# Performance work log

Hardware: AMD Instinct MI355X
Metric: run time of the kernel (lower is better)

Reference implementation:

```python
import jax, jax.numpy as jnp
import numpy as np

EMB = 1024
HEADS = 16
HEAD_DIM = EMB // HEADS
EPS = 1e-5


def setup_inputs() -> dict:
    key = jax.random.key(0)
    ks = jax.random.split(key, 10)
    B, T, D = 2, 2048, EMB
    s = 1.0 / np.sqrt(D)
    inp = {
        "x": jax.random.normal(ks[0], (B, T, D), dtype=jnp.float32),
        "wq": jax.random.normal(ks[1], (D, D), dtype=jnp.float32) * s,
        "bq": jnp.zeros((D,), jnp.float32),
        "wk": jax.random.normal(ks[2], (D, D), dtype=jnp.float32) * s,
        "bk": jnp.zeros((D,), jnp.float32),
        "wv": jax.random.normal(ks[3], (D, D), dtype=jnp.float32) * s,
        "bv": jnp.zeros((D,), jnp.float32),
        "wo": jax.random.normal(ks[4], (D, D), dtype=jnp.float32) * s,
        "bo": jnp.zeros((D,), jnp.float32),
        "gamma": jnp.ones((D,), jnp.float32),
        "beta": jnp.zeros((D,), jnp.float32),
    }
    return inp


def _attention(x, wq, bq, wk, bk, wv, bv, wo, bo, gamma, beta):
    B, T, D = x.shape
    H, Hd = HEADS, HEAD_DIM
    q = (x @ wq + bq).reshape(B, T, H, Hd)
    k = (x @ wk + bk).reshape(B, T, H, Hd)
    v = (x @ wv + bv).reshape(B, T, H, Hd)
    # scores: [B, H, T, T]
    scores = jnp.einsum("bthd,bshd->bhts", q, k) / np.sqrt(Hd)
    attn = jax.nn.softmax(scores, axis=-1)  # dropout is identity in eval
    ctx = jnp.einsum("bhts,bshd->bthd", attn, v).reshape(B, T, D)
    out = ctx @ wo + bo
    y = x + out  # residual (dropout identity)
    mu = jnp.mean(y, axis=-1, keepdims=True)
    var = jnp.var(y, axis=-1, keepdims=True)
    return (y - mu) * jax.lax.rsqrt(var + EPS) * gamma + beta


def reference(x, wq, bq, wk, bk, wv, bv, wo, bo, gamma, beta):
    return _attention(x, wq, bq, wk, bk, wv, bv, wo, bo, gamma, beta)
```

## Files before the change

kernel.cpp:

```cpp
#include <hip/hip_runtime.h>

#define BSZ   2
#define TSEQ  2048
#define DMOD  1024
#define NHEAD 16
#define HDIM  64
#define MROW  (BSZ*TSEQ)
#define LNEPS 1e-5f
#define QSCALE 0.18033688011f

typedef __bf16 bf16x8 __attribute__((ext_vector_type(8)));
typedef float  f32x4  __attribute__((ext_vector_type(4)));
typedef unsigned short us8 __attribute__((ext_vector_type(8)));
typedef unsigned short us4 __attribute__((ext_vector_type(4)));

__device__ __forceinline__ unsigned short f2bf(float f) {
    unsigned u = __float_as_uint(f);
    u += 0x7FFF + ((u >> 16) & 1);
    return (unsigned short)(u >> 16);
}
__device__ __forceinline__ float bf2f(unsigned short u) {
    return __uint_as_float((unsigned)u << 16);
}

__device__ __forceinline__ float fexp2(float x) {
#if __has_builtin(__builtin_amdgcn_exp2f)
    return __builtin_amdgcn_exp2f(x);
#else
    return __expf(x * 0.6931471805599453f);
#endif
}

__device__ __forceinline__ void gld_lds16(const void* g, void* l) {
    __builtin_amdgcn_global_load_lds(
        (const __attribute__((address_space(1))) unsigned int*)g,
        (__attribute__((address_space(3))) unsigned int*)l, 16, 0, 0);
}

__global__ __launch_bounds__(256) void prep_k(
    const float* __restrict__ x,
    const float* __restrict__ wq, const float* __restrict__ wk,
    const float* __restrict__ wv, const float* __restrict__ wo,
    unsigned short* __restrict__ Xb,
    unsigned short* __restrict__ WqkvT, unsigned short* __restrict__ WoT)
{
    const int tid = threadIdx.x;
    if (blockIdx.x < 2048) {
        const size_t i = ((size_t)blockIdx.x * 256 + tid) * 8;
        float4 a = *(const float4*)&x[i];
        float4 b = *(const float4*)&x[i + 4];
        union { unsigned short u[8]; uint4 v; } o;
        o.u[0]=f2bf(a.x); o.u[1]=f2bf(a.y); o.u[2]=f2bf(a.z); o.u[3]=f2bf(a.w);
        o.u[4]=f2bf(b.x); o.u[5]=f2bf(b.y); o.u[6]=f2bf(b.z); o.u[7]=f2bf(b.w);
        *(uint4*)&Xb[i] = o.v;
        return;
    }
    __shared__ float T[64][68];
    const int id = blockIdx.x - 2048;
    const int z  = id >> 8;
    const int bx = id & 15;
    const int by = (id >> 4) & 15;
    const float* W = (z == 0) ? wq : (z == 1) ? wk : (z == 2) ? wv : wo;
    unsigned short* Wt = (z < 3) ? (WqkvT + (size_t)z*1024*1024) : WoT;
    const int lr = tid >> 4, lc = (tid & 15) * 4;
    #pragma unroll
    for (int p = 0; p < 4; ++p) {
        const int kk = p*16 + lr;
        float4 v = *(const float4*)&W[(size_t)(by*64 + kk)*1024 + bx*64 + lc];
        T[lc+0][kk] = v.x; T[lc+1][kk] = v.y; T[lc+2][kk] = v.z; T[lc+3][kk] = v.w;
    }
    __syncthreads();
    #pragma unroll
    for (int p = 0; p < 2; ++p) {
        const int nl = p*32 + (tid >> 3);
        const int kb = (tid & 7) * 8;
        float4 a = *(const float4*)&T[nl][kb];
        float4 b = *(const float4*)&T[nl][kb+4];
        union { unsigned short u[8]; uint4 v; } o;
        o.u[0]=f2bf(a.x); o.u[1]=f2bf(a.y); o.u[2]=f2bf(a.z); o.u[3]=f2bf(a.w);
        o.u[4]=f2bf(b.x); o.u[5]=f2bf(b.y); o.u[6]=f2bf(b.z); o.u[7]=f2bf(b.w);
        *(uint4*)&Wt[(size_t)(bx*64 + nl)*1024 + by*64 + kb] = o.v;
    }
}

#define PH_SYNC() do { __builtin_amdgcn_s_barrier(); \
    asm volatile("s_waitcnt lgkmcnt(0)" ::: "memory"); \
    __builtin_amdgcn_sched_barrier(0); } while (0)

template<int N>
__device__ __forceinline__ void vmwait() {
    if constexpr (N == 0)      asm volatile("s_waitcnt vmcnt(0)" ::: "memory");
    else if constexpr (N == 3) asm volatile("s_waitcnt vmcnt(3)" ::: "memory");
    else                       asm volatile("s_waitcnt vmcnt(4)" ::: "memory");
}

template<int NB>
struct CoreT {
    const unsigned short *sA, *sB;
    unsigned short *A0w, *A1w, *B0w, *B1w;
    const unsigned short *fA0, *fA1, *fB0, *fB1;
    int swz0, swz1;
};

__device__ __forceinline__ void stageA4(const unsigned short* s, unsigned short* d) {
    #pragma unroll
    for (int u = 0; u < 4; ++u) gld_lds16(s + u*64*1024, d + u*4096);
}
template<int NB>
__device__ __forceinline__ void stageBall(const unsigned short* s, unsigned short* d) {
    #pragma unroll
    for (int u = 0; u < NB; ++u) gld_lds16(s + u*64*1024, d + u*4096);
}
__device__ __forceinline__ void stageB01(const unsigned short* s, unsigned short* d) {
    gld_lds16(s, d); gld_lds16(s + 64*1024, d + 4096);
}
template<int NB>
__device__ __forceinline__ void stageBrest(const unsigned short* s, unsigned short* d) {
    #pragma unroll
    for (int u = 2; u < NB; ++u) gld_lds16(s + u*64*1024, d + u*4096);
}

template<int NB>
__device__ __forceinline__ void core_setup(CoreT<NB>& C, unsigned short* LDS,
    const unsigned short* A, const unsigned short* Bt, int bm, int bn, int kbase)
{
    const int tid = threadIdx.x;
    const int w = tid >> 6, lane = tid & 63;
    const int quad = lane >> 4, l16 = lane & 15;
    const int wm = w >> 2, wn = w & 3;
    const int r_l = lane >> 3, c_l = lane & 7;
    C.sA = A  + (size_t)(bm + w*8 + r_l)*1024 + (c_l ^ r_l)*8 + kbase;
    C.sB = Bt + (size_t)(bn + w*8 + r_l)*1024 + (c_l ^ r_l)*8 + kbase;
    unsigned short* A0 = LDS;
    unsigned short* A1 = LDS + 16384;
    unsigned short* B0 = LDS + 32768;
    unsigned short* B1 = B0 + NB*4096;
    C.A0w = A0 + w*512; C.A1w = A1 + w*512;
    C.B0w = B0 + w*512; C.B1w = B1 + w*512;
    C.fA0 = A0 + (wm*128 + l16)*64; C.fA1 = A1 + (wm*128 + l16)*64;
    C.fB0 = B0 + (wn*NB*16 + l16)*64;  C.fB1 = B1 + (wn*NB*16 + l16)*64;
    C.swz0 = ( quad      ^ (l16 & 7)) * 8;
    C.swz1 = ((4 + quad) ^ (l16 & 7)) * 8;
}

template<int NB>
__device__ __forceinline__ void ld_b(const CoreT<NB>& C, bf16x8 (&bfr)[NB][2],
                                     const unsigned short* fB) {
    #pragma unroll
    for (int n = 0; n < NB; ++n) {
        bfr[n][0] = *(const bf16x8*)(fB + n*1024 + C.swz0);
        bfr[n][1] = *(const bf16x8*)(fB + n*1024 + C.swz1);
    }
}

template<int Q, int NB>
__device__ __forceinline__ void ld_a(const CoreT<NB>& C, bf16x8 (&af)[2][2],
                                     const unsigned short* fA) {
    #pragma unroll
    for (int dm = 0; dm < 2; ++dm) {
        af[dm][0] = *(const bf16x8*)(fA + (Q*2+dm)*1024 + C.swz0);
        af[dm][1] = *(const bf16x8*)(fA + (Q*2+dm)*1024 + C.swz1);
    }
}

template<int Q, int NB>
__device__ __forceinline__ void mma_q(f32x4 (&acc)[8][NB], bf16x8 (&af)[2][2],
                                      bf16x8 (&bfr)[NB][2]) {
    __builtin_amdgcn_s_setprio(1);
    #pragma unroll
    for (int dm = 0; dm < 2; ++dm)
        #pragma unroll
        for (int n = 0; n < NB; ++n) {
            f32x4 t = acc[Q*2+dm][n];
            t = __builtin_amdgcn_mfma_f32_16x16x32_bf16(af[dm][0], bfr[n][0], t, 0, 0, 0);
            t = __builtin_amdgcn_mfma_f32_16x16x32_bf16(af[dm][1], bfr[n][1], t, 0, 0, 0);
            acc[Q*2+dm][n] = t;
        }
    __builtin_amdgcn_s_setprio(0);
}

template<int NIT, int NB>
__device__ __forceinline__ void core_kloop(const CoreT<NB>& C, f32x4 (&acc)[8][NB])
{
    stageA4(C.sA, C.A0w);
    stageBall<NB>(C.sB,      C.B0w);
    stageBall<NB>(C.sB + 64, C.B1w);
    vmwait<NB>();
    __builtin_amdgcn_s_barrier();

    bf16x8 bfr[NB][2];
    bf16x8 af[2][2];

    #pragma unroll 1
    for (int it = 0; it < NIT - 1; ++it) {
        const int kk = it * 128;
        ld_b<NB>(C, bfr, C.fB0);
        ld_a<0,NB>(C, af, C.fA0);
        stageA4(C.sA + kk + 64, C.A1w);
        PH_SYNC();  mma_q<0,NB>(acc, af, bfr);
        __builtin_amdgcn_s_barrier();
        ld_a<1,NB>(C, af, C.fA0);
        stageB01(C.sB + kk + 128, C.B0w);
        PH_SYNC();  mma_q<1,NB>(acc, af, bfr);
        __builtin_amdgcn_s_barrier();
        ld_a<2,NB>(C, af, C.fA0);
        stageBrest<NB>(C.sB + kk + 128, C.B0w);
        PH_SYNC();  mma_q<2,NB>(acc, af, bfr);
        __builtin_amdgcn_s_barrier();
        ld_a<3,NB>(C, af, C.fA0);
        PH_SYNC();  mma_q<3,NB>(acc, af, bfr);
        vmwait<NB>();
        __builtin_amdgcn_s_barrier();
        ld_b<NB>(C, bfr, C.fB1);
        ld_a<0,NB>(C, af, C.fA1);
        stageA4(C.sA + kk + 128, C.A0w);
        PH_SYNC();  mma_q<0,NB>(acc, af, bfr);
        __builtin_amdgcn_s_barrier();
        ld_a<1,NB>(C, af, C.fA1);
        stageB01(C.sB + kk + 192, C.B1w);
        PH_SYNC();  mma_q<1,NB>(acc, af, bfr);
        __builtin_amdgcn_s_barrier();
        ld_a<2,NB>(C, af, C.fA1);
        stageBrest<NB>(C.sB + kk + 192, C.B1w);
        PH_SYNC();  mma_q<2,NB>(acc, af, bfr);
        __builtin_amdgcn_s_barrier();
        ld_a<3,NB>(C, af, C.fA1);
        PH_SYNC();  mma_q<3,NB>(acc, af, bfr);
        vmwait<NB>();
        __builtin_amdgcn_s_barrier();
    }
    {
        const int kk = (NIT - 1) * 128;
        ld_b<NB>(C, bfr, C.fB0);
        ld_a<0,NB>(C, af, C.fA0);
        stageA4(C.sA + kk + 64, C.A1w);
        PH_SYNC();  mma_q<0,NB>(acc, af, bfr);
        __builtin_amdgcn_s_barrier();
        ld_a<1,NB>(C, af, C.fA0); PH_SYNC(); mma_q<1,NB>(acc, af, bfr); __builtin_amdgcn_s_barrier();
        ld_a<2,NB>(C, af, C.fA0); PH_SYNC(); mma_q<2,NB>(acc, af, bfr); __builtin_amdgcn_s_barrier();
        ld_a<3,NB>(C, af, C.fA0); PH_SYNC(); mma_q<3,NB>(acc, af, bfr);
        vmwait<0>();
        __builtin_amdgcn_s_barrier();
        ld_b<NB>(C, bfr, C.fB1);
        ld_a<0,NB>(C, af, C.fA1); PH_SYNC(); mma_q<0,NB>(acc, af, bfr); __builtin_amdgcn_s_barrier();
        ld_a<1,NB>(C, af, C.fA1); PH_SYNC(); mma_q<1,NB>(acc, af, bfr); __builtin_amdgcn_s_barrier();
        ld_a<2,NB>(C, af, C.fA1); PH_SYNC(); mma_q<2,NB>(acc, af, bfr); __builtin_amdgcn_s_barrier();
        ld_a<3,NB>(C, af, C.fA1); PH_SYNC(); mma_q<3,NB>(acc, af, bfr);
    }
}

__global__ __launch_bounds__(512, 1) void gemm_qkv_k(
    const unsigned short* __restrict__ A, const unsigned short* __restrict__ Bt,
    const float* __restrict__ b0, const float* __restrict__ b1,
    const float* __restrict__ b2,
    unsigned short* __restrict__ oQ, unsigned short* __restrict__ oK,
    unsigned short* __restrict__ oV)
{
    extern __shared__ unsigned short LDS[];
    const int ob = blockIdx.x;
    const int wg = (ob & 7) * 32 + (ob >> 3);
    const int by = wg >> 4, bx = wg & 15;
    const int bm = by * 256, bn = bx * 192;

    CoreT<3> C;
    core_setup<3>(C, LDS, A, Bt, bm, bn, 0);

    f32x4 acc[8][3];
    #pragma unroll
    for (int i = 0; i < 8; ++i)
        #pragma unroll
        for (int j = 0; j < 3; ++j) acc[i][j] = (f32x4){0.f,0.f,0.f,0.f};

    core_kloop<8,3>(C, acc);

    const int tid = threadIdx.x;
    const int w = tid >> 6, lane = tid & 63;
    const int quad = lane >> 4, l16 = lane & 15;
    const int wm = w >> 2, wn = w & 3;
    #pragma unroll
    for (int n = 0; n < 3; ++n) {
        const int c0  = bn + wn*48 + n*16;
        const int seg = c0 >> 10;
        const int cl0 = c0 & 1023;
        if (seg < 2) {
            unsigned short* O = (seg == 0) ? oQ : oK;
            const float sc = (seg == 0) ? QSCALE : 1.0f;
            const float* bias = (seg == 0) ? b0 : b1;
            const int col = cl0 + l16;
            const float bs = bias[col];
            #pragma unroll
            for (int m = 0; m < 8; ++m)
                #pragma unroll
                for (int r = 0; r < 4; ++r) {
                    const int grow = bm + wm*128 + m*16 + quad*4 + r;
                    O[(size_t)grow*1024 + col] = f2bf((acc[m][n][r] + bs) * sc);
                }
        } else {
            const int ch = cl0 + l16;
            const float bs = b2[ch];
            #pragma unroll
            for (int m = 0; m < 8; ++m) {
                const int grow0 = bm + wm*128 + m*16 + quad*4;
                us4 o;
                #pragma unroll
                for (int r = 0; r < 4; ++r) o[r] = f2bf(acc[m][n][r] + bs);
                *(us4*)&oV[(size_t)ch*MROW + grow0] = o;
            }
        }
    }
}

struct CoreP {
    const unsigned short *sA, *sB;
    unsigned short *A0w, *A1w, *B0w, *B1w;
    const unsigned short *fA0, *fA1, *fB0, *fB1;
    int swz0, swz1;
};

__device__ __forceinline__ void stage4p(const unsigned short* s, unsigned short* d) {
    #pragma unroll
    for (int u = 0; u < 4; ++u) gld_lds16(s + u*32*1024, d + u*2048);
}
__device__ __forceinline__ void stage01p(const unsigned short* s, unsigned short* d) {
    gld_lds16(s, d); gld_lds16(s + 32*1024, d + 2048);
}
__device__ __forceinline__ void stage23p(const unsigned short* s, unsigned short* d) {
    gld_lds16(s + 2*32*1024, d + 2*2048); gld_lds16(s + 3*32*1024, d + 3*2048);
}

__device__ __forceinline__ void corep_setup(CoreP& C, unsigned short* LDS,
    const unsigned short* A, const unsigned short* Bt, int bm, int bn, int kbase)
{
    const int tid = threadIdx.x;
    const int w = tid >> 6, lane = tid & 63;
    const int quad = lane >> 4, l16 = lane & 15;
    const int wm = w >> 1, wn = w & 1;
    const int r_l = lane >> 3, c_l = lane & 7;
    C.sA = A  + (size_t)(bm + w*8 + r_l)*1024 + (c_l ^ r_l)*8 + kbase;
    C.sB = Bt + (size_t)(bn + w*8 + r_l)*1024 + (c_l ^ r_l)*8 + kbase;
    unsigned short* A0 = LDS;
    unsigned short* A1 = LDS + 8192;
    unsigned short* B0 = LDS + 16384;
    unsigned short* B1 = LDS + 24576;
    C.A0w = A0 + w*512; C.A1w = A1 + w*512;
    C.B0w = B0 + w*512; C.B1w = B1 + w*512;
    C.fA0 = A0 + (wm*64 + l16)*64; C.fA1 = A1 + (wm*64 + l16)*64;
    C.fB0 = B0 + (wn*64 + l16)*64; C.fB1 = B1 + (wn*64 + l16)*64;
    C.swz0 = ( quad      ^ (l16 & 7)) * 8;
    C.swz1 = ((4 + quad) ^ (l16 & 7)) * 8;
}

__device__ __forceinline__ void ld_bp(const CoreP& C, bf16x8 (&bfr)[4][2],
                                      const unsigned short* fB) {
    #pragma unroll
    for (int n = 0; n < 4; ++n) {
        bfr[n][0] = *(const bf16x8*)(fB + n*1024 + C.swz0);
        bfr[n][1] = *(const bf16x8*)(fB + n*1024 + C.swz1);
    }
}
template<int Q>
__device__ __forceinline__ void ld_ap(const CoreP& C, bf16x8 (&af)[2],
                                      const unsigned short* fA) {
    af[0] = *(const bf16x8*)(fA + Q*1024 + C.swz0);
    af[1] = *(const bf16x8*)(fA + Q*1024 + C.swz1);
}
template<int Q>
__device__ __forceinline__ void mma_p(f32x4 (&acc)[4][4], bf16x8 (&af)[2],
                                      bf16x8 (&bfr)[4][2]) {
    __builtin_amdgcn_s_setprio(1);
    #pragma unroll
    for (int n = 0; n < 4; ++n) {
        f32x4 t = acc[Q][n];
        t = __builtin_amdgcn_mfma_f32_16x16x32_bf16(af[0], bfr[n][0], t, 0, 0, 0);
        t = __builtin_amdgcn_mfma_f32_16x16x32_bf16(af[1], bfr[n][1], t, 0, 0, 0);
        acc[Q][n] = t;
    }
    __builtin_amdgcn_s_setprio(0);
}

template<int NIT>
__device__ __forceinline__ void corep_kloop(const CoreP& C, f32x4 (&acc)[4][4])
{
    stage4p(C.sA, C.A0w);
    stage4p(C.sB, C.B0w);
    stage4p(C.sB + 64, C.B1w);
    vmwait<4>();
    __builtin_amdgcn_s_barrier();

    bf16x8 bfr[4][2];
    bf16x8 af[2];

    #pragma unroll 1
    for (int it = 0; it < NIT - 1; ++it) {
        const int kk = it * 128;
        ld_bp(C, bfr, C.fB0);
        ld_ap<0>(C, af, C.fA0);
        stage4p(C.sA + kk + 64, C.A1w);
        PH_SYNC();  mma_p<0>(acc, af, bfr);
        __builtin_amdgcn_s_barrier();
        ld_ap<1>(C, af, C.fA0);
        stage01p(C.sB + kk + 128, C.B0w);
        PH_SYNC();  mma_p<1>(acc, af, bfr);
        __builtin_amdgcn_s_barrier();
        ld_ap<2>(C, af, C.fA0);
        stage23p(C.sB + kk + 128, C.B0w);
        PH_SYNC();  mma_p<2>(acc, af, bfr);
        __builtin_amdgcn_s_barrier();
        ld_ap<3>(C, af, C.fA0);
        PH_SYNC();  mma_p<3>(acc, af, bfr);
        vmwait<4>();
        __builtin_amdgcn_s_barrier();
        ld_bp(C, bfr, C.fB1);
        ld_ap<0>(C, af, C.fA1);
        stage4p(C.sA + kk + 128, C.A0w);
        PH_SYNC();  mma_p<0>(acc, af, bfr);
        __builtin_amdgcn_s_barrier();
        ld_ap<1>(C, af, C.fA1);
        stage01p(C.sB + kk + 192, C.B1w);
        PH_SYNC();  mma_p<1>(acc, af, bfr);
        __builtin_amdgcn_s_barrier();
        ld_ap<2>(C, af, C.fA1);
        stage23p(C.sB + kk + 192, C.B1w);
        PH_SYNC();  mma_p<2>(acc, af, bfr);
        __builtin_amdgcn_s_barrier();
        ld_ap<3>(C, af, C.fA1);
        PH_SYNC();  mma_p<3>(acc, af, bfr);
        vmwait<4>();
        __builtin_amdgcn_s_barrier();
    }
    {
        const int kk = (NIT - 1) * 128;
        ld_bp(C, bfr, C.fB0);
        ld_ap<0>(C, af, C.fA0);
        stage4p(C.sA + kk + 64, C.A1w);
        PH_SYNC();  mma_p<0>(acc, af, bfr);
        __builtin_amdgcn_s_barrier();
        ld_ap<1>(C, af, C.fA0); PH_SYNC(); mma_p<1>(acc, af, bfr); __builtin_amdgcn_s_barrier();
        ld_ap<2>(C, af, C.fA0); PH_SYNC(); mma_p<2>(acc, af, bfr); __builtin_amdgcn_s_barrier();
        ld_ap<3>(C, af, C.fA0); PH_SYNC(); mma_p<3>(acc, af, bfr);
        vmwait<0>();
        __builtin_amdgcn_s_barrier();
        ld_bp(C, bfr, C.fB1);
        ld_ap<0>(C, af, C.fA1); PH_SYNC(); mma_p<0>(acc, af, bfr); __builtin_amdgcn_s_barrier();
        ld_ap<1>(C, af, C.fA1); PH_SYNC(); mma_p<1>(acc, af, bfr); __builtin_amdgcn_s_barrier();
        ld_ap<2>(C, af, C.fA1); PH_SYNC(); mma_p<2>(acc, af, bfr); __builtin_amdgcn_s_barrier();
        ld_ap<3>(C, af, C.fA1); PH_SYNC(); mma_p<3>(acc, af, bfr);
    }
}

__global__ __launch_bounds__(256, 2) void gemm_proj_k(
    const unsigned short* __restrict__ A, const unsigned short* __restrict__ Bt,
    unsigned short* __restrict__ P)
{
    extern __shared__ unsigned short LDS[];
    const int ob = blockIdx.x;
    const int wg = (ob & 7) * 32 + (ob >> 3);
    const int by = wg >> 3, bx = wg & 7;
    const int kz = blockIdx.y;
    const int bm = by * 128, bn = bx * 128;

    CoreP C;
    corep_setup(C, LDS, A, Bt, bm, bn, kz * 512);

    f32x4 acc[4][4];
    #pragma unroll
    for (int i = 0; i < 4; ++i)
        #pragma unroll
        for (int j = 0; j < 4; ++j) acc[i][j] = (f32x4){0.f,0.f,0.f,0.f};

    corep_kloop<4>(C, acc);

    const int tid = threadIdx.x;
    const int w = tid >> 6, lane = tid & 63;
    const int quad = lane >> 4, l16 = lane & 15;
    const int wm = w >> 1, wn = w & 1;
    unsigned short* O = P + (size_t)kz*MROW*1024;
    #pragma unroll
    for (int n = 0; n < 4; ++n) {
        const int col = bn + wn*64 + n*16 + l16;
        #pragma unroll
        for (int m = 0; m < 4; ++m)
            #pragma unroll
            for (int r = 0; r < 4; ++r) {
                const int grow = bm + wm*64 + m*16 + quad*4 + r;
                O[(size_t)grow*1024 + col] = f2bf(acc[m][n][r]);
            }
    }
}

__global__ __launch_bounds__(256, 4) void attn_k(
    const unsigned short* __restrict__ Qg,
    const unsigned short* __restrict__ Kg,
    const unsigned short* __restrict__ Vtg,
    unsigned short* __restrict__ CTX)
{
    extern __shared__ __align__(16) char lds_raw[];
    unsigned short* Ks = (unsigned short*)lds_raw;
    unsigned short* Vs = (unsigned short*)(lds_raw + 8192);
    unsigned short* Qs = (unsigned short*)lds_raw;
    float* Od = (float*)lds_raw;
    float* Ld = (float*)(lds_raw + 17408);

    const int tid  = threadIdx.x;
    const int wv   = tid >> 6;
    const int lane = tid & 63;
    const int quad = lane >> 4;
    const int l16  = lane & 15;
    const int wq   = wv & 1;
    const int wk   = wv >> 1;

    const int n    = blockIdx.x;
    const int slot = n >> 3;
    const int grp  = (n & 7) + 8 * (slot >> 5);
    const int qx   = slot & 31;
    const int h    = grp >> 1;
    const int b    = grp & 1;
    const int qb   = qx * 64;

    {
        const int r  = tid >> 2;
        const int cb = (tid & 3) * 16;
        const unsigned short* Qrow = Qg + ((size_t)(b*TSEQ + qb + r))*DMOD + h*HDIM + cb;
        *(us8*)&Qs[r*72 + cb]     = *(const us8*)&Qrow[0];
        *(us8*)&Qs[r*72 + cb + 8] = *(const us8*)&Qrow[8];
    }
    __syncthreads();
    bf16x8 qf[2][2];
    #pragma unroll
    for (int nt = 0; nt < 2; ++nt)
        #pragma unroll
        for (int kh = 0; kh < 2; ++kh)
            qf[nt][kh] = *(const bf16x8*)&Qs[(wq*32 + nt*16 + l16)*72 + kh*32 + quad*8];
    __syncthreads();

    const int sr = lane >> 3;
    const int sc = lane & 7;
    const bool isK = (wv < 2);
    const int part = wv & 1;
    const unsigned short* gbase;
    unsigned int goff[4];
    unsigned short* ldst;
    if (isK) {
        gbase = Kg + ((size_t)(b*TSEQ))*DMOD + h*HDIM;
        #pragma unroll
        for (int s = 0; s < 4; ++s) {
            const int R = part*32 + s*8 + sr;
            const int gc = sc ^ ((R ^ (R >> 2)) & 7);
            goff[s] = (unsigned)(R*DMOD + gc*8);
        }
        ldst = Ks + part*2048;
    } else {
        gbase = Vtg + ((size_t)(h*HDIM))*MROW + b*TSEQ;
        #pragma unroll
        for (int s = 0; s < 4; ++s) {
            const int D = part*32 + s*8 + sr;
            const int gc = sc ^ (D & 7);
            goff[s] = (unsigned)(D*MROW + gc*8);
        }
        ldst = Vs + part*2048;
    }
    const size_t gstep = isK ? (size_t)64*DMOD : (size_t)64;

    const int rowA_l = (l16 >> 2)*8 + (l16 & 3);
    const int rA = wk*32 + rowA_l;
    const int rB = rA + 4;
    const int swA = ((rA ^ (rA >> 2)) & 7);
    const int swB = ((rB ^ (rB >> 2)) & 7);
    const unsigned short* kA0 = &Ks[rA*64 + ( quad      ^ swA)*8];
    const unsigned short* kA1 = &Ks[rA*64 + ((4 + quad) ^ swA)*8];
    const unsigned short* kB0 = &Ks[rB*64 + ( quad      ^ swB)*8];
    const unsigned short* kB1 = &Ks[rB*64 + ((4 + quad) ^ swB)*8];
    const unsigned short* vp[4];
    #pragma unroll
    for (int dt = 0; dt < 4; ++dt)
        vp[dt] = &Vs[(dt*16 + l16)*64 + ((wk*4 + quad) ^ (l16 & 7))*8];

    bf16x8 onef;
    { union { unsigned short u[8]; bf16x8 v; } o1;
      #pragma unroll
      for (int i = 0; i < 8; ++i) o1.u[i] = 0x3F80;
      onef = o1.v; }

    f32x4 oacc[4][2];
    f32x4 lacc[2];
    #pragma unroll
    for (int dt = 0; dt < 4; ++dt)
        #pragma unroll
        for (int nt = 0; nt < 2; ++nt) oacc[dt][nt] = (f32x4){0.f,0.f,0.f,0.f};
    lacc[0] = (f32x4){0.f,0.f,0.f,0.f};
    lacc[1] = (f32x4){0.f,0.f,0.f,0.f};

    #pragma unroll 1
    for (int it = 0; it < 32; ++it) {
        __syncthreads();
        #pragma unroll
        for (int s = 0; s < 4; ++s)
            gld_lds16(gbase + (size_t)it*gstep + goff[s], ldst + s*512);
        __syncthreads();

        bf16x8 ka0 = *(const bf16x8*)kA0;
        bf16x8 ka1 = *(const bf16x8*)kA1;
        bf16x8 kb0 = *(const bf16x8*)kB0;
        bf16x8 kb1 = *(const bf16x8*)kB1;
        bf16x8 vf[4];
        #pragma unroll
        for (int dt = 0; dt < 4; ++dt) vf[dt] = *(const bf16x8*)vp[dt];

        bf16x8 pf[2];
        #pragma unroll
        for (int nt = 0; nt < 2; ++nt) {
            f32x4 z = (f32x4){0.f,0.f,0.f,0.f};
            z = __builtin_amdgcn_mfma_f32_16x16x32_bf16(ka0, qf[nt][0], z, 0, 0, 0);
            f32x4 sA = __builtin_amdgcn_mfma_f32_16x16x32_bf16(ka1, qf[nt][1], z, 0, 0, 0);
            f32x4 z2 = (f32x4){0.f,0.f,0.f,0.f};
            z2 = __builtin_amdgcn_mfma_f32_16x16x32_bf16(kb0, qf[nt][0], z2, 0, 0, 0);
            f32x4 sB = __builtin_amdgcn_mfma_f32_16x16x32_bf16(kb1, qf[nt][1], z2, 0, 0, 0);
            float eA[4], eB[4];
            #pragma unroll
            for (int r = 0; r < 4; ++r) { eA[r] = fexp2(sA[r]); eB[r] = fexp2(sB[r]); }
            union { unsigned d[4]; bf16x8 v; } up;
            up.d[0] = __builtin_amdgcn_perm(__float_as_uint(eA[1]), __float_as_uint(eA[0]), 0x07060302);
            up.d[1] = __builtin_amdgcn_perm(__float_as_uint(eA[3]), __float_as_uint(eA[2]), 0x07060302);
            up.d[2] = __builtin_amdgcn_perm(__float_as_uint(eB[1]), __float_as_uint(eB[0]), 0x07060302);
            up.d[3] = __builtin_amdgcn_perm(__float_as_uint(eB[3]), __float_as_uint(eB[2]), 0x07060302);
            pf[nt] = up.v;
        }
        __builtin_amdgcn_s_setprio(1);
        #pragma unroll
        for (int nt = 0; nt < 2; ++nt) {
            lacc[nt] = __builtin_amdgcn_mfma_f32_16x16x32_bf16(onef, pf[nt], lacc[nt], 0, 0, 0);
            #pragma unroll
            for (int dt = 0; dt < 4; ++dt)
                oacc[dt][nt] = __builtin_amdgcn_mfma_f32_16x16x32_bf16(vf[dt], pf[nt], oacc[dt][nt], 0, 0, 0);
        }
        __builtin_amdgcn_s_setprio(0);
    }

    __syncthreads();
    if (wk == 0) {
        float* od = Od + wq*32*68;
        #pragma unroll
        for (int nt = 0; nt < 2; ++nt) {
            #pragma unroll
            for (int dt = 0; dt < 4; ++dt)
                *(f32x4*)&od[(nt*16 + l16)*68 + dt*16 + quad*4] = oacc[dt][nt];
            if (quad == 0) Ld[wq*32 + nt*16 + l16] = lacc[nt][0];
        }
    }
    __syncthreads();
    if (wk == 1) {
        const float* od = Od + wq*32*68;
        #pragma unroll
        for (int nt = 0; nt < 2; ++nt) {
            const float l = Ld[wq*32 + nt*16 + l16] + lacc[nt][0];
            const float inv = 1.f / l;
            const int q = qb + wq*32 + nt*16 + l16;
            unsigned short* crow = CTX + ((size_t)(b*TSEQ + q))*DMOD + h*HDIM;
            #pragma unroll
            for (int dt = 0; dt < 4; ++dt) {
                f32x4 p = *(const f32x4*)&od[(nt*16 + l16)*68 + dt*16 + quad*4];
                us4 o;
                #pragma unroll
                for (int r = 0; r < 4; ++r) o[r] = f2bf((p[r] + oacc[dt][nt][r]) * inv);
                *(us4*)&crow[dt*16 + quad*4] = o;
            }
        }
    }
}

__global__ __launch_bounds__(256) void red_ln_k(
    const float* __restrict__ x, const unsigned short* __restrict__ P,
    const float* __restrict__ bo,
    const float* __restrict__ gamma, const float* __restrict__ beta,
    float* __restrict__ out)
{
    __shared__ float rs[4], rss[4];
    const int row = blockIdx.x;
    const int tid = threadIdx.x;
    const int c = tid * 4;
    const float4 xv = *(const float4*)&x[(size_t)row*DMOD + c];
    const us4 p0 = *(const us4*)&P[(size_t)row*DMOD + c];
    const us4 p1 = *(const us4*)&P[(size_t)(MROW + row)*DMOD + c];
    const float4 bv4 = *(const float4*)&bo[c];
    const float v0 = xv.x + bf2f(p0[0]) + bf2f(p1[0]) + bv4.x;
    const float v1 = xv.y + bf2f(p0[1]) + bf2f(p1[1]) + bv4.y;
    const float v2 = xv.z + bf2f(p0[2]) + bf2f(p1[2]) + bv4.z;
    const float v3 = xv.w + bf2f(p0[3]) + bf2f(p1[3]) + bv4.w;
    float s  = v0 + v1 + v2 + v3;
    float ss = v0*v0 + v1*v1 + v2*v2 + v3*v3;
    #pragma unroll
    for (int o = 32; o > 0; o >>= 1) {
        s  += __shfl_down(s,  o, 64);
        ss += __shfl_down(ss, o, 64);
    }
    if ((tid & 63) == 0) { rs[tid >> 6] = s; rss[tid >> 6] = ss; }
    __syncthreads();
    s  = rs[0] + rs[1] + rs[2] + rs[3];
    ss = rss[0] + rss[1] + rss[2] + rss[3];
    const float mean = s * (1.f/DMOD);
    const float var  = ss * (1.f/DMOD) - mean*mean;
    const float rstd = rsqrtf(var + LNEPS);
    const float4 gv = *(const float4*)&gamma[c];
    const float4 bv = *(const float4*)&beta[c];
    float4 o;
    o.x = (v0 - mean)*rstd*gv.x + bv.x;
    o.y = (v1 - mean)*rstd*gv.y + bv.y;
    o.z = (v2 - mean)*rstd*gv.z + bv.z;
    o.w = (v3 - mean)*rstd*gv.w + bv.w;
    *(float4*)&out[(size_t)row*DMOD + c] = o;
}

extern "C" void kernel_launch(void* const* d_in, const int* in_sizes, int n_in,
                              void* d_out, int out_size, void* d_ws, size_t ws_size,
                              hipStream_t stream) {
    const float* x     = (const float*)d_in[0];
    const float* wq    = (const float*)d_in[1];
    const float* bq    = (const float*)d_in[2];
    const float* wk    = (const float*)d_in[3];
    const float* bk    = (const float*)d_in[4];
    const float* wvp   = (const float*)d_in[5];
    const float* bvp   = (const float*)d_in[6];
    const float* wo    = (const float*)d_in[7];
    const float* bo    = (const float*)d_in[8];
    const float* gamma = (const float*)d_in[9];
    const float* beta  = (const float*)d_in[10];
    float* out = (float*)d_out;

    unsigned short* Xb    = (unsigned short*)d_ws;
    unsigned short* WqkvT = Xb    + (size_t)MROW*DMOD;
    unsigned short* WoT   = WqkvT + (size_t)3072*1024;
    unsigned short* Qb    = WoT   + (size_t)1024*1024;
    unsigned short* Kb    = Qb    + (size_t)MROW*DMOD;
    unsigned short* VtG   = Kb    + (size_t)MROW*DMOD;
    unsigned short* CTXb  = VtG   + (size_t)DMOD*MROW;
    unsigned short* Pp    = CTXb  + (size_t)MROW*DMOD;

    prep_k<<<3072, 256, 0, stream>>>(x, wq, wk, wvp, wo, Xb, WqkvT, WoT);

    gemm_qkv_k<<<dim3(256), 512, 114688, stream>>>(
        Xb, WqkvT, bq, bk, bvp, Qb, Kb, VtG);

    attn_k<<<dim3(1024), 256, 17664, stream>>>(Qb, Kb, VtG, CTXb);

    gemm_proj_k<<<dim3(256, 2), 256, 65536, stream>>>(CTXb, WoT, Pp);

    red_ln_k<<<MROW, 256, 0, stream>>>(x, Pp, bo, gamma, beta, out);
}
```

Measured before the change: 192.8 us.

## Double-buffer K/V loads in attention kernel with 128-query tiles and split-key waves

Restructures the attention kernel so each block processes 128 queries instead of 64 and loads 128 keys per iteration (two 64-key halves, one per wave pair), with the K/V tiles double-buffered in 64KB of LDS so the next tile's global-to-LDS copy overlaps compute. The grid becomes a 3D (query-tile, head, batch) launch and occupancy is lowered to 2 blocks per CU. The aim is to hide global load latency, remove one barrier per iteration and raise Q reuse per K/V tile. The cost is higher register pressure from 4x4 accumulators and fewer resident blocks, plus the loss of the previous block-index swizzle that grouped blocks for L2 reuse.

```diff
diff --git a/kernel.cpp b/kernel.cpp
--- a/kernel.cpp
+++ b/kernel.cpp
@@ -488,18 +488,17 @@
     }
 }
 
-__global__ __launch_bounds__(256, 4) void attn_k(
+__global__ __launch_bounds__(256, 2) void attn_k(
     const unsigned short* __restrict__ Qg,
     const unsigned short* __restrict__ Kg,
     const unsigned short* __restrict__ Vtg,
     unsigned short* __restrict__ CTX)
 {
     extern __shared__ __align__(16) char lds_raw[];
-    unsigned short* Ks = (unsigned short*)lds_raw;
-    unsigned short* Vs = (unsigned short*)(lds_raw + 8192);
+    unsigned short* KV = (unsigned short*)lds_raw;
     unsigned short* Qs = (unsigned short*)lds_raw;
     float* Od = (float*)lds_raw;
-    float* Ld = (float*)(lds_raw + 17408);
+    float* Ld = (float*)(lds_raw + 65536);
 
     const int tid  = threadIdx.x;
     const int wv   = tid >> 6;
@@ -508,72 +507,58 @@
     const int l16  = lane & 15;
     const int wq   = wv & 1;
     const int wk   = wv >> 1;
-
-    const int n    = blockIdx.x;
-    const int slot = n >> 3;
-    const int grp  = (n & 7) + 8 * (slot >> 5);
-    const int qx   = slot & 31;
-    const int h    = grp >> 1;
-    const int b    = grp & 1;
-    const int qb   = qx * 64;
+    const int qb   = blockIdx.x * 128;
+    const int h    = blockIdx.y;
+    const int b    = blockIdx.z;
 
     {
-        const int r  = tid >> 2;
-        const int cb = (tid & 3) * 16;
-        const unsigned short* Qrow = Qg + ((size_t)(b*TSEQ + qb + r))*DMOD + h*HDIM + cb;
-        *(us8*)&Qs[r*72 + cb]     = *(const us8*)&Qrow[0];
-        *(us8*)&Qs[r*72 + cb + 8] = *(const us8*)&Qrow[8];
+        const int row = tid & 127, cb = (tid >> 7) * 32;
+        const unsigned short* Qrow = Qg + ((size_t)(b*TSEQ + qb + row))*DMOD + h*HDIM + cb;
+        #pragma unroll
+        for (int j = 0; j < 4; ++j)
+            *(us8*)&Qs[row*72 + cb + j*8] = *(const us8*)&Qrow[j*8];
     }
     __syncthreads();
-    bf16x8 qf[2][2];
-    #pragma unroll
-    for (int nt = 0; nt < 2; ++nt)
+    bf16x8 qf[4][2];
+    #pragma unroll
+    for (int nt = 0; nt < 4; ++nt)
         #pragma unroll
         for (int kh = 0; kh < 2; ++kh)
-            qf[nt][kh] = *(const bf16x8*)&Qs[(wq*32 + nt*16 + l16)*72 + kh*32 + quad*8];
+            qf[nt][kh] = *(const bf16x8*)&Qs[(wq*64 + nt*16 + l16)*72 + kh*32 + quad*8];
     __syncthreads();
 
     const int sr = lane >> 3;
     const int sc = lane & 7;
     const bool isK = (wv < 2);
-    const int part = wv & 1;
+    const int half = wv & 1;
     const unsigned short* gbase;
-    unsigned int goff[4];
-    unsigned short* ldst;
+    unsigned int goff[8];
+    unsigned short* ldstb;
     if (isK) {
-        gbase = Kg + ((size_t)(b*TSEQ))*DMOD + h*HDIM;
-        #pragma unroll
-        for (int s = 0; s < 4; ++s) {
-            const int R = part*32 + s*8 + sr;
+        gbase = Kg + ((size_t)(b*TSEQ + half*1024))*DMOD + h*HDIM;
+        #pragma unroll
+        for (int s = 0; s < 8; ++s) {
+            const int R = s*8 + sr;
             const int gc = sc ^ ((R ^ (R >> 2)) & 7);
             goff[s] = (unsigned)(R*DMOD + gc*8);
         }
-        ldst = Ks + part*2048;
+        ldstb = KV + half*4096;
     } else {
-        gbase = Vtg + ((size_t)(h*HDIM))*MROW + b*TSEQ;
-        #pragma unroll
-        for (int s = 0; s < 4; ++s) {
-            const int D = part*32 + s*8 + sr;
+        gbase = Vtg + ((size_t)(h*HDIM))*MROW + b*TSEQ + half*1024;
+        #pragma unroll
+        for (int s = 0; s < 8; ++s) {
+            const int D = s*8 + sr;
             const int gc = sc ^ (D & 7);
             goff[s] = (unsigned)(D*MROW + gc*8);
         }
-        ldst = Vs + part*2048;
+        ldstb = KV + 16384 + half*4096;
     }
     const size_t gstep = isK ? (size_t)64*DMOD : (size_t)64;
 
     const int rowA_l = (l16 >> 2)*8 + (l16 & 3);
-    const int rA = wk*32 + rowA_l;
-    const int rB = rA + 4;
-    const int swA = ((rA ^ (rA >> 2)) & 7);
-    const int swB = ((rB ^ (rB >> 2)) & 7);
-    const unsigned short* kA0 = &Ks[rA*64 + ( quad      ^ swA)*8];
-    const unsigned short* kA1 = &Ks[rA*64 + ((4 + quad) ^ swA)*8];
-    const unsigned short* kB0 = &Ks[rB*64 + ( quad      ^ swB)*8];
-    const unsigned short* kB1 = &Ks[rB*64 + ((4 + quad) ^ swB)*8];
-    const unsigned short* vp[4];
-    #pragma unroll
-    for (int dt = 0; dt < 4; ++dt)
-        vp[dt] = &Vs[(dt*16 + l16)*64 + ((wk*4 + quad) ^ (l16 & 7))*8];
+    const int rowB_l = rowA_l + 4;
+    const int swA = (rowA_l ^ (rowA_l >> 2)) & 7;
+    const int swB = (rowB_l ^ (rowB_l >> 2)) & 7;
 
     bf16x8 onef;
     { union { unsigned short u[8]; bf16x8 v; } o1;
@@ -581,80 +566,100 @@
       for (int i = 0; i < 8; ++i) o1.u[i] = 0x3F80;
       onef = o1.v; }
 
-    f32x4 oacc[4][2];
-    f32x4 lacc[2];
+    f32x4 oacc[4][4];
+    f32x4 lacc[4];
     #pragma unroll
     for (int dt = 0; dt < 4; ++dt)
         #pragma unroll
-        for (int nt = 0; nt < 2; ++nt) oacc[dt][nt] = (f32x4){0.f,0.f,0.f,0.f};
-    lacc[0] = (f32x4){0.f,0.f,0.f,0.f};
-    lacc[1] = (f32x4){0.f,0.f,0.f,0.f};
-
-    #pragma unroll 1
-    for (int it = 0; it < 32; ++it) {
+        for (int nt = 0; nt < 4; ++nt) oacc[dt][nt] = (f32x4){0.f,0.f,0.f,0.f};
+    #pragma unroll
+    for (int nt = 0; nt < 4; ++nt) lacc[nt] = (f32x4){0.f,0.f,0.f,0.f};
+
+    #pragma unroll
+    for (int s = 0; s < 8; ++s)
+        gld_lds16(gbase + goff[s], ldstb + s*512);
+    __syncthreads();
+
+    for (int it = 0; it < 16; ++it) {
+        const int cbuf = (it & 1) * 8192;
+        if (it < 15) {
+            const unsigned short* gn = gbase + (size_t)(it+1)*gstep;
+            unsigned short* d = ldstb + (cbuf ^ 8192);
+            #pragma unroll
+            for (int s = 0; s < 8; ++s)
+                gld_lds16(gn + goff[s], d + s*512);
+        }
+        __builtin_amdgcn_sched_barrier(0);
+        const unsigned short* KsW = KV + cbuf + wk*4096;
+        const unsigned short* VsW = KV + 16384 + cbuf + wk*4096;
+
+        #pragma unroll
+        for (int gl = 0; gl < 2; ++gl) {
+            const int rA = gl*32 + rowA_l;
+            const int rB = gl*32 + rowB_l;
+            bf16x8 ka0 = *(const bf16x8*)&KsW[rA*64 + ((quad     ^ swA))*8];
+            bf16x8 ka1 = *(const bf16x8*)&KsW[rA*64 + (((4+quad) ^ swA))*8];
+            bf16x8 kb0 = *(const bf16x8*)&KsW[rB*64 + ((quad     ^ swB))*8];
+            bf16x8 kb1 = *(const bf16x8*)&KsW[rB*64 + (((4+quad) ^ swB))*8];
+            bf16x8 vf[4];
+            #pragma unroll
+            for (int dt = 0; dt < 4; ++dt)
+                vf[dt] = *(const bf16x8*)&VsW[(dt*16 + l16)*64 + ((gl*4 + quad) ^ (l16 & 7))*8];
+
+            f32x4 sA[4], sB[4];
+            #pragma unroll
+            for (int nt = 0; nt < 4; ++nt) {
+                f32x4 z = (f32x4){0.f,0.f,0.f,0.f};
+                z = __builtin_amdgcn_mfma_f32_16x16x32_bf16(ka0, qf[nt][0], z, 0, 0, 0);
+                sA[nt] = __builtin_amdgcn_mfma_f32_16x16x32_bf16(ka1, qf[nt][1], z, 0, 0, 0);
+                f32x4 z2 = (f32x4){0.f,0.f,0.f,0.f};
+                z2 = __builtin_amdgcn_mfma_f32_16x16x32_bf16(kb0, qf[nt][0], z2, 0, 0, 0);
+                sB[nt] = __builtin_amdgcn_mfma_f32_16x16x32_bf16(kb1, qf[nt][1], z2, 0, 0, 0);
+            }
+            bf16x8 pf[4];
+            #pragma unroll
+            for (int nt = 0; nt < 4; ++nt) {
+                float eA[4], eB[4];
+                #pragma unroll
+                for (int r = 0; r < 4; ++r) { eA[r] = fexp2(sA[nt][r]); eB[r] = fexp2(sB[nt][r]); }
+                union { unsigned d[4]; bf16x8 v; } up;
+                up.d[0] = __builtin_amdgcn_perm(__float_as_uint(eA[1]), __float_as_uint(eA[0]), 0x07060302);
+                up.d[1] = __builtin_amdgcn_perm(__float_as_uint(eA[3]), __float_as_uint(eA[2]), 0x07060302);
+                up.d[2] = __builtin_amdgcn_perm(__float_as_uint(eB[1]), __float_as_uint(eB[0]), 0x07060302);
+                up.d[3] = __builtin_amdgcn_perm(__float_as_uint(eB[3]), __float_as_uint(eB[2]), 0x07060302);
+                pf[nt] = up.v;
+            }
+            __builtin_amdgcn_s_setprio(1);
+            #pragma unroll
+            for (int nt = 0; nt < 4; ++nt) {
+                lacc[nt] = __builtin_amdgcn_mfma_f32_16x16x32_bf16(onef, pf[nt], lacc[nt], 0, 0, 0);
+                #pragma unroll
+                for (int dt = 0; dt < 4; ++dt)
+                    oacc[dt][nt] = __builtin_amdgcn_mfma_f32_16x16x32_bf16(vf[dt], pf[nt], oacc[dt][nt], 0, 0, 0);
+            }
+            __builtin_amdgcn_s_setprio(0);
+        }
         __syncthreads();
-        #pragma unroll
-        for (int s = 0; s < 4; ++s)
-            gld_lds16(gbase + (size_t)it*gstep + goff[s], ldst + s*512);
-        __syncthreads();
-
-        bf16x8 ka0 = *(const bf16x8*)kA0;
-        bf16x8 ka1 = *(const bf16x8*)kA1;
-        bf16x8 kb0 = *(const bf16x8*)kB0;
-        bf16x8 kb1 = *(const bf16x8*)kB1;
-        bf16x8 vf[4];
-        #pragma unroll
-        for (int dt = 0; dt < 4; ++dt) vf[dt] = *(const bf16x8*)vp[dt];
-
-        bf16x8 pf[2];
-        #pragma unroll
-        for (int nt = 0; nt < 2; ++nt) {
-            f32x4 z = (f32x4){0.f,0.f,0.f,0.f};
-            z = __builtin_amdgcn_mfma_f32_16x16x32_bf16(ka0, qf[nt][0], z, 0, 0, 0);
-            f32x4 sA = __builtin_amdgcn_mfma_f32_16x16x32_bf16(ka1, qf[nt][1], z, 0, 0, 0);
-            f32x4 z2 = (f32x4){0.f,0.f,0.f,0.f};
-            z2 = __builtin_amdgcn_mfma_f32_16x16x32_bf16(kb0, qf[nt][0], z2, 0, 0, 0);
-            f32x4 sB = __builtin_amdgcn_mfma_f32_16x16x32_bf16(kb1, qf[nt][1], z2, 0, 0, 0);
-            float eA[4], eB[4];
-            #pragma unroll
-            for (int r = 0; r < 4; ++r) { eA[r] = fexp2(sA[r]); eB[r] = fexp2(sB[r]); }
-            union { unsigned d[4]; bf16x8 v; } up;
-            up.d[0] = __builtin_amdgcn_perm(__float_as_uint(eA[1]), __float_as_uint(eA[0]), 0x07060302);
-            up.d[1] = __builtin_amdgcn_perm(__float_as_uint(eA[3]), __float_as_uint(eA[2]), 0x07060302);
-            up.d[2] = __builtin_amdgcn_perm(__float_as_uint(eB[1]), __float_as_uint(eB[0]), 0x07060302);
-            up.d[3] = __builtin_amdgcn_perm(__float_as_uint(eB[3]), __float_as_uint(eB[2]), 0x07060302);
-            pf[nt] = up.v;
-        }
-        __builtin_amdgcn_s_setprio(1);
-        #pragma unroll
-        for (int nt = 0; nt < 2; ++nt) {
-            lacc[nt] = __builtin_amdgcn_mfma_f32_16x16x32_bf16(onef, pf[nt], lacc[nt], 0, 0, 0);
-            #pragma unroll
-            for (int dt = 0; dt < 4; ++dt)
-                oacc[dt][nt] = __builtin_amdgcn_mfma_f32_16x16x32_bf16(vf[dt], pf[nt], oacc[dt][nt], 0, 0, 0);
-        }
-        __builtin_amdgcn_s_setprio(0);
-    }
-
-    __syncthreads();
+    }
+
     if (wk == 0) {
-        float* od = Od + wq*32*68;
-        #pragma unroll
-        for (int nt = 0; nt < 2; ++nt) {
+        float* od = Od + wq*64*68;
+        #pragma unroll
+        for (int nt = 0; nt < 4; ++nt) {
             #pragma unroll
             for (int dt = 0; dt < 4; ++dt)
                 *(f32x4*)&od[(nt*16 + l16)*68 + dt*16 + quad*4] = oacc[dt][nt];
-            if (quad == 0) Ld[wq*32 + nt*16 + l16] = lacc[nt][0];
+            if (quad == 0) Ld[wq*64 + nt*16 + l16] = lacc[nt][0];
         }
     }
     __syncthreads();
     if (wk == 1) {
-        const float* od = Od + wq*32*68;
-        #pragma unroll
-        for (int nt = 0; nt < 2; ++nt) {
-            const float l = Ld[wq*32 + nt*16 + l16] + lacc[nt][0];
+        const float* od = Od + wq*64*68;
+        #pragma unroll
+        for (int nt = 0; nt < 4; ++nt) {
+            const float l = Ld[wq*64 + nt*16 + l16] + lacc[nt][0];
             const float inv = 1.f / l;
-            const int q = qb + wq*32 + nt*16 + l16;
+            const int q = qb + wq*64 + nt*16 + l16;
             unsigned short* crow = CTX + ((size_t)(b*TSEQ + q))*DMOD + h*HDIM;
             #pragma unroll
             for (int dt = 0; dt < 4; ++dt) {
@@ -740,7 +745,7 @@
     gemm_qkv_k<<<dim3(256), 512, 114688, stream>>>(
         Xb, WqkvT, bq, bk, bvp, Qb, Kb, VtG);
 
-    attn_k<<<dim3(1024), 256, 17664, stream>>>(Qb, Kb, VtG, CTXb);
+    attn_k<<<dim3(TSEQ/128, NHEAD, BSZ), 256, 66048, stream>>>(Qb, Kb, VtG, CTXb);
 
     gemm_proj_k<<<dim3(256, 2), 256, 65536, stream>>>(CTXb, WoT, Pp);
 
```

Result: no change. 190.1 us (-1.4%).
